# Performance work log

Hardware: AMD Instinct MI355X
Metric: run time of the kernel (lower is better)

The kernel has to match this reference:

```python
import jax, jax.numpy as jnp
import numpy as np

D = 300   # hidden dim (Linear(300,300))
L = 160   # seq len, forced by W3 = Linear(160,1)


def _linear(x, W, b):
    # torch Linear: x @ W.T + b, W is (out, in)
    return jnp.matmul(x, W.T) + b


def setup_inputs() -> dict:
    key = jax.random.key(0)
    ks = jax.random.split(key, 16)
    B = 1024
    s = 1.0 / np.sqrt(D)
    inp = {
        'T_feature': jax.random.normal(ks[0], (B, L, D), jnp.float32),
        'CD_feature': jax.random.normal(ks[1], (B, L, D), jnp.float32),
        'Wproj': jax.random.normal(ks[2], (D, D), jnp.float32) * s,
        'bproj': jnp.zeros((D,), jnp.float32),
        'WqT_w': jax.random.normal(ks[3], (D, D), jnp.float32) * s,
        'WqT_b': jnp.zeros((D,), jnp.float32),
        'WqCD_w': jax.random.normal(ks[4], (D, D), jnp.float32) * s,
        'WqCD_b': jnp.zeros((D,), jnp.float32),
        'WkT_w': jax.random.normal(ks[5], (D, D), jnp.float32) * s,
        'WkT_b': jnp.zeros((D,), jnp.float32),
        'WkCD_w': jax.random.normal(ks[6], (D, D), jnp.float32) * s,
        'WkCD_b': jnp.zeros((D,), jnp.float32),
        'W3_w': jax.random.normal(ks[7], (1, L), jnp.float32) * (1.0 / np.sqrt(L)),
        'W3_b': jnp.zeros((1,), jnp.float32),
    }
    return inp


def reference(T_feature, CD_feature, Wproj, bproj, WqT_w, WqT_b, WqCD_w, WqCD_b,
              WkT_w, WkT_b, WkCD_w, WkCD_b, W3_w, W3_b):
    sqrt_d = jnp.sqrt(jnp.float32(D))
    proj_T = _linear(T_feature, Wproj, bproj)     # (B, L, D)
    proj_CD = _linear(CD_feature, Wproj, bproj)   # (B, L, D)

    # N_tensor @ proj_T is just the mean over tokens (weights 1/Len)
    mean_T = jnp.mean(proj_T, axis=1, keepdims=True)          # (B, 1, D)
    qT = _linear(mean_T, WqT_w, WqT_b)                        # (B, 1, D)
    kT = _linear(proj_T, WkT_w, WkT_b)                        # (B, L, D)
    alphaT = jnp.einsum('bqd,bkd->bqk', qT, kT) / sqrt_d      # (B, 1, L)
    ZT = jax.nn.sigmoid(alphaT)

    qCD = _linear(proj_CD, WqCD_w, WqCD_b)                    # (B, L, D)
    kCD = _linear(proj_CD, WkCD_w, WkCD_b)                    # (B, L, D)
    alphaCD = jnp.einsum('bqd,bkd->bqk', qCD, kCD) / sqrt_d   # (B, L, L)
    ZCD = jax.nn.sigmoid(alphaCD)

    # The per-token loop+cat is a plain broadcast multiply: Mt[:,i,:] = ZCD[:,i,:] * ZT[:,0,:]
    Mt = ZCD * ZT                                             # (B, L, L)
    alpha_f = jax.nn.softmax(_linear(Mt, W3_w, W3_b), axis=1) # (B, L, 1)

    # Second loop is a per-token scalar scale: HCD[:,i,:] = alpha_f[:,i,0] * proj_CD[:,i,:]
    HCD = alpha_f * proj_CD                                   # (B, L, D)
    return (proj_T, HCD)
```

## Files before the change

### kernel.cpp

```cpp
#include <hip/hip_runtime.h>
#include <hip/hip_bf16.h>


typedef __attribute__((ext_vector_type(8))) short short8;
typedef __attribute__((ext_vector_type(4))) float f32x4;

#define DP 320

__device__ __forceinline__ unsigned short f2bf(float x) {
  unsigned int u = __builtin_bit_cast(unsigned int, x);
  u += 0x7FFFu + ((u >> 16) & 1u);
  return (unsigned short)(u >> 16);
}
__device__ __forceinline__ float bf2f(unsigned short h) {
  unsigned int u = ((unsigned int)h) << 16;
  return __builtin_bit_cast(float, u);
}
__device__ __forceinline__ void gload16(const void* g, void* l) {
  __builtin_amdgcn_global_load_lds(
      (const __attribute__((address_space(1))) unsigned int*)g,
      (__attribute__((address_space(3))) unsigned int*)l, 16, 0, 0);
}
__device__ __forceinline__ float sigm(float x) { return 1.0f / (1.0f + __expf(-x)); }

__global__ void wb_k(const float* __restrict__ W, unsigned short* __restrict__ Wb) {
  int n = blockIdx.x, k = threadIdx.x;
  unsigned short v = 0;
  if (n < 300 && k < 300) v = f2bf(W[n * 300 + k]);
  Wb[n * DP + k] = v;
}

__global__ void crossdot_k(const float* __restrict__ Wa, const float* __restrict__ ba,
                           const float* __restrict__ Wc, const float* __restrict__ bc,
                           unsigned short* __restrict__ out_h, float* __restrict__ out_f,
                           float scale) {
  int n = blockIdx.x, c = threadIdx.x;
  float v = 0.f;
  if (n <= 300 && c <= 300) {
    for (int o = 0; o < 300; ++o) {
      float a = (c < 300) ? Wa[o * 300 + c] : ba[o];
      float b = (n < 300) ? Wc[o * 300 + n] : bc[o];
      v += a * b;
    }
    v *= scale;
  }
  if (out_h) out_h[n * DP + c] = f2bf(v);
  else       out_f[n * DP + c] = v;
}

template<int MODE>
__global__ __launch_bounds__(512)
void gemm_k(const float* __restrict__ Af, const unsigned short* __restrict__ Ah,
            const unsigned short* __restrict__ Bsrc, const float* __restrict__ bias,
            float* __restrict__ Of, unsigned short* __restrict__ Oh) {
  __shared__ __align__(16) unsigned short As[2][256 * 32];
  __shared__ __align__(16) unsigned short Bs[2][160 * 32];
  const int tid = threadIdx.x;
  const int wid = tid >> 6, lane = tid & 63;
  const long m0 = (long)blockIdx.y * 256;
  const int n0 = blockIdx.x * 160;

  f32x4 acc[4][5];
#pragma unroll
  for (int i = 0; i < 4; ++i)
#pragma unroll
    for (int j = 0; j < 5; ++j) acc[i][j] = (f32x4){0.f, 0.f, 0.f, 0.f};

  auto stageA = [&](int buf, int k0) {
    if (MODE < 2) {
#pragma unroll
      for (int it = 0; it < 2; ++it) {
        const int row = (tid >> 2) + it * 128;
        const int cg = (tid & 3) * 8;
        const float* p = Af + (m0 + row) * 300 + k0 + cg;
        short8 h;
        if (k0 + cg + 7 < 300) {
          f32x4 x0 = *(const f32x4*)p;
          f32x4 x1 = *(const f32x4*)(p + 4);
#pragma unroll
          for (int j = 0; j < 4; ++j) {
            h[j] = (short)f2bf(x0[j]);
            h[j + 4] = (short)f2bf(x1[j]);
          }
        } else {
#pragma unroll
          for (int j = 0; j < 8; ++j) {
            float v = (k0 + cg + j < 300) ? p[j] : 0.f;
            h[j] = (short)f2bf(v);
          }
        }
        *(short8*)&As[buf][row * 32 + cg] = h;
      }
    } else {
#pragma unroll
      for (int c = 0; c < 2; ++c) {
        int ch = wid + c * 8;
        int f = ch * 512 + lane * 8;
        gload16(Ah + (m0 + (f >> 5)) * DP + k0 + (f & 31), &As[buf][ch * 512]);
      }
    }
  };
  auto stageB = [&](int buf, int k0) {
    {
      int f = wid * 512 + lane * 8;
      gload16(Bsrc + (n0 + (f >> 5)) * DP + k0 + (f & 31), &Bs[buf][wid * 512]);
    }
    if (wid < 2) {
      int ch = wid + 8;
      int f = ch * 512 + lane * 8;
      gload16(Bsrc + (n0 + (f >> 5)) * DP + k0 + (f & 31), &Bs[buf][ch * 512]);
    }
  };

  stageA(0, 0);
  stageB(0, 0);
  __syncthreads();
  int buf = 0;
  const int rm = (wid >> 1) * 64, cn = (wid & 1) * 80;
  const int lr = lane & 15, lk = (lane >> 4) * 8;
  for (int kc = 0; kc < 10; ++kc) {
    if (kc < 9) { stageA(buf ^ 1, (kc + 1) * 32); stageB(buf ^ 1, (kc + 1) * 32); }
    short8 a[4], bb[5];
#pragma unroll
    for (int mf = 0; mf < 4; ++mf)
      a[mf] = *(const short8*)&As[buf][(rm + mf * 16 + lr) * 32 + lk];
#pragma unroll
    for (int nf = 0; nf < 5; ++nf)
      bb[nf] = *(const short8*)&Bs[buf][(cn + nf * 16 + lr) * 32 + lk];
#pragma unroll
    for (int mf = 0; mf < 4; ++mf)
#pragma unroll
      for (int nf = 0; nf < 5; ++nf)
        acc[mf][nf] = __builtin_amdgcn_mfma_f32_16x16x32_bf16(a[mf], bb[nf], acc[mf][nf], 0, 0, 0);
    __syncthreads();
    buf ^= 1;
  }

#pragma unroll
  for (int mf = 0; mf < 4; ++mf) {
#pragma unroll
    for (int nf = 0; nf < 5; ++nf) {
      const int col = n0 + cn + nf * 16 + lr;
      float bv = 0.f;
      if (MODE < 2 && col < 300) bv = bias[col];
#pragma unroll
      for (int r = 0; r < 4; ++r) {
        const long row = m0 + rm + mf * 16 + (lane >> 4) * 4 + r;
        float v = acc[mf][nf][r] + bv;
        if (MODE == 0) {
          if (col < 300) Of[row * 300 + col] = v;
        } else if (MODE == 1) {
          unsigned short u = (col < 300) ? f2bf(v)
                            : ((col == 300) ? f2bf(1.0f) : (unsigned short)0);
          Oh[row * DP + col] = u;
        } else {
          Oh[row * DP + col] = (col <= 300) ? f2bf(v) : (unsigned short)0;
        }
      }
    }
  }
}

__global__ void mean_k(const float* __restrict__ projT, float* __restrict__ meanT) {
  int b = blockIdx.x, tid = threadIdx.x;
  const float* p = projT + (size_t)b * 48000;
  for (int c = tid; c < 300; c += 256) {
    float s = 0.f;
    for (int l = 0; l < 160; ++l) s += p[l * 300 + c];
    meanT[b * DP + c] = s * (1.0f / 160.0f);
  }
}

__global__ __launch_bounds__(320)
void vt_k(const float* __restrict__ Pmat, const float* __restrict__ meanT,
          float* __restrict__ vT, float* __restrict__ cT) {
  __shared__ float mt[300];
  int b = blockIdx.x, tid = threadIdx.x;
  if (tid < 300) mt[tid] = meanT[b * DP + tid];
  __syncthreads();
  if (tid <= 300) {
    float s = 0.f;
    for (int a = 0; a < 300; ++a) s += Pmat[a * DP + tid] * mt[a];
    s += Pmat[300 * DP + tid];
    if (tid < 300) vT[b * DP + tid] = s;
    else cT[b] = s;
  }
}

__global__ __launch_bounds__(256)
void zt_k(const float* __restrict__ projT, const float* __restrict__ vT,
          const float* __restrict__ cT, float* __restrict__ ZT) {
  __shared__ float v[304];
  int b = blockIdx.x, tid = threadIdx.x, wid = tid >> 6, lane = tid & 63;
  for (int c = tid; c < 300; c += 256) v[c] = vT[b * DP + c];
  if (tid == 0) v[300] = cT[b];
  __syncthreads();
  const float* p = projT + (size_t)b * 48000;
  for (int j = wid; j < 160; j += 4) {
    const float* row = p + j * 300;
    float s = 0.f;
    for (int c = lane; c < 300; c += 64) s += v[c] * row[c];
#pragma unroll
    for (int m = 1; m < 64; m <<= 1) s += __shfl_xor(s, m, 64);
    if (lane == 0) ZT[b * 160 + j] = sigm(s + v[300]);
  }
}

__global__ __launch_bounds__(320)
void finale_k(const unsigned short* __restrict__ Y, const unsigned short* __restrict__ P,
              const float* __restrict__ ZT, const float* __restrict__ W3w,
              float* __restrict__ out) {
  __shared__ __align__(16) unsigned short Ys[2][160 * 32];
  __shared__ __align__(16) unsigned short Ps[2][160 * 32];
  __shared__ float t_arr[160];
  __shared__ float s_arr[160];
  __shared__ float red0;

  const int b = blockIdx.x;
  const int tid = threadIdx.x, wid = tid >> 6, lane = tid & 63;
  const unsigned short* Yb = Y + (size_t)b * 160 * DP;
  const unsigned short* Pb = P + (size_t)b * 160 * DP;

  if (tid < 160) t_arr[tid] = ZT[b * 160 + tid] * W3w[tid];

  auto stage = [&](int buf, int k0) {
#pragma unroll
    for (int c = 0; c < 2; ++c) {
      int ch = wid + c * 5;
      int f = ch * 512 + lane * 8;
      int ro = (f >> 5) * DP + k0 + (f & 31);
      gload16(Yb + ro, &Ys[buf][ch * 512]);
      gload16(Pb + ro, &Ps[buf][ch * 512]);
    }
  };

  f32x4 acc[2][10];
#pragma unroll
  for (int i = 0; i < 2; ++i)
#pragma unroll
    for (int j = 0; j < 10; ++j) acc[i][j] = (f32x4){0.f, 0.f, 0.f, 0.f};

  stage(0, 0);
  __syncthreads();
  int buf = 0;
  const int lr = lane & 15, lk = (lane >> 4) * 8;
  const int rm = wid * 32;
  for (int kc = 0; kc < 10; ++kc) {
    if (kc < 9) stage(buf ^ 1, (kc + 1) * 32);
    short8 a[2], bb[10];
#pragma unroll
    for (int mf = 0; mf < 2; ++mf)
      a[mf] = *(const short8*)&Ys[buf][(rm + mf * 16 + lr) * 32 + lk];
#pragma unroll
    for (int nf = 0; nf < 10; ++nf)
      bb[nf] = *(const short8*)&Ps[buf][(nf * 16 + lr) * 32 + lk];
#pragma unroll
    for (int mf = 0; mf < 2; ++mf)
#pragma unroll
      for (int nf = 0; nf < 10; ++nf)
        acc[mf][nf] = __builtin_amdgcn_mfma_f32_16x16x32_bf16(a[mf], bb[nf], acc[mf][nf], 0, 0, 0);
    __syncthreads();
    buf ^= 1;
  }

  float tv[10];
#pragma unroll
  for (int nf = 0; nf < 10; ++nf) tv[nf] = t_arr[nf * 16 + lr];
  float rp[2][4];
#pragma unroll
  for (int mf = 0; mf < 2; ++mf)
#pragma unroll
    for (int r = 0; r < 4; ++r) {
      float s = 0.f;
#pragma unroll
      for (int nf = 0; nf < 10; ++nf) s += sigm(acc[mf][nf][r]) * tv[nf];
      rp[mf][r] = s;
    }
#pragma unroll
  for (int m = 1; m < 16; m <<= 1)
#pragma unroll
    for (int mf = 0; mf < 2; ++mf)
#pragma unroll
      for (int r = 0; r < 4; ++r) rp[mf][r] += __shfl_xor(rp[mf][r], m, 64);
  if (lr == 0) {
#pragma unroll
    for (int mf = 0; mf < 2; ++mf)
#pragma unroll
      for (int r = 0; r < 4; ++r)
        s_arr[rm + mf * 16 + (lane >> 4) * 4 + r] = rp[mf][r];
  }
  __syncthreads();
  if (wid == 0) {
    float v0 = s_arr[lane], v1 = s_arr[lane + 64];
    float v2 = (lane < 32) ? s_arr[lane + 128] : -3.0e38f;
    float mx = fmaxf(fmaxf(v0, v1), v2);
#pragma unroll
    for (int m = 1; m < 64; m <<= 1) mx = fmaxf(mx, __shfl_xor(mx, m, 64));
    float e0 = __expf(v0 - mx), e1 = __expf(v1 - mx);
    float e2 = (lane < 32) ? __expf(v2 - mx) : 0.f;
    s_arr[lane] = e0; s_arr[lane + 64] = e1;
    if (lane < 32) s_arr[lane + 128] = e2;
    float sm = e0 + e1 + e2;
#pragma unroll
    for (int m = 1; m < 64; m <<= 1) sm += __shfl_xor(sm, m, 64);
    if (lane == 0) red0 = 1.0f / sm;
  }
  __syncthreads();
  const float inv = red0;
  float* ob = out + (size_t)b * 48000;
  for (int e = tid; e < 48000; e += 320) {
    const int i = e / 300;
    const int c = e - i * 300;
    ob[e] = s_arr[i] * inv * bf2f(Pb[i * DP + c]);
  }
}

extern "C" void kernel_launch(void* const* d_in, const int* in_sizes, int n_in,
                              void* d_out, int out_size, void* d_ws, size_t ws_size,
                              hipStream_t stream) {
  (void)in_sizes; (void)n_in; (void)out_size; (void)ws_size;
  const float* T      = (const float*)d_in[0];
  const float* CD     = (const float*)d_in[1];
  const float* Wproj  = (const float*)d_in[2];
  const float* bproj  = (const float*)d_in[3];
  const float* WqT_w  = (const float*)d_in[4];
  const float* WqT_b  = (const float*)d_in[5];
  const float* WqCD_w = (const float*)d_in[6];
  const float* WqCD_b = (const float*)d_in[7];
  const float* WkT_w  = (const float*)d_in[8];
  const float* WkT_b  = (const float*)d_in[9];
  const float* WkCD_w = (const float*)d_in[10];
  const float* WkCD_b = (const float*)d_in[11];
  const float* W3_w   = (const float*)d_in[12];

  char* ws = (char*)d_ws;
  size_t off = 0;
  auto alloc = [&](size_t bytes) { void* p = ws + off; off = (off + bytes + 255) & ~(size_t)255; return p; };
  unsigned short* pCD   = (unsigned short*)alloc((size_t)1024 * 160 * DP * 2);
  unsigned short* Yb    = (unsigned short*)alloc((size_t)1024 * 160 * DP * 2);
  unsigned short* Wb    = (unsigned short*)alloc((size_t)DP * DP * 2);
  unsigned short* MaugT = (unsigned short*)alloc((size_t)DP * DP * 2);
  float* Pmat  = (float*)alloc((size_t)DP * DP * 4);
  float* meanT = (float*)alloc((size_t)1024 * DP * 4);
  float* vT    = (float*)alloc((size_t)1024 * DP * 4);
  float* cT    = (float*)alloc((size_t)1024 * 4);
  float* ZT    = (float*)alloc((size_t)1024 * 160 * 4);

  float* projT = (float*)d_out;
  float* HCD   = (float*)d_out + (size_t)49152000;

  const float isd = 1.0f / sqrtf(300.0f);

  wb_k<<<dim3(320), dim3(320), 0, stream>>>(Wproj, Wb);
  crossdot_k<<<dim3(320), dim3(320), 0, stream>>>(WqCD_w, WqCD_b, WkCD_w, WkCD_b, MaugT, nullptr, isd);
  crossdot_k<<<dim3(320), dim3(320), 0, stream>>>(WkT_w, WkT_b, WqT_w, WqT_b, nullptr, Pmat, isd);

  gemm_k<0><<<dim3(2, 640), dim3(512), 0, stream>>>(T,  nullptr, Wb, bproj, projT, nullptr);
  gemm_k<1><<<dim3(2, 640), dim3(512), 0, stream>>>(CD, nullptr, Wb, bproj, nullptr, pCD);

  mean_k<<<dim3(1024), dim3(256), 0, stream>>>(projT, meanT);
  vt_k<<<dim3(1024), dim3(320), 0, stream>>>(Pmat, meanT, vT, cT);
  zt_k<<<dim3(1024), dim3(256), 0, stream>>>(projT, vT, cT, ZT);

  gemm_k<2><<<dim3(2, 640), dim3(512), 0, stream>>>(nullptr, pCD, MaugT, nullptr, nullptr, Yb);

  finale_k<<<dim3(1024), dim3(320), 0, stream>>>(Yb, pCD, ZT, W3_w, HCD);
}
```

Before: 773.7 us.

## Fuse Y=P·M GEMM into finale, merge projection GEMMs and gate kernels

Drops the separate gemm_k<2> that wrote Y (bf16 pCD·Maug) to global memory. finale_k now keeps the whole per-batch pCD tile in swizzled LDS and computes Y in chunks on the fly before the second MFMA, which removes a large global write and re-read. The two projection GEMMs are merged into one launch that covers the full N=320 width per block with padded LDS rows. mean, vT and ZT are fused into a single gate_k. The cost is heavy LDS use (~130KB) in finale and lower occupancy, plus redundant recomputation of the Maug operand loads per batch.

```diff
diff --git a/kernel.cpp b/kernel.cpp
--- a/kernel.cpp
+++ b/kernel.cpp
@@ -22,6 +22,8 @@
       (__attribute__((address_space(3))) unsigned int*)l, 16, 0, 0);
 }
 __device__ __forceinline__ float sigm(float x) { return 1.0f / (1.0f + __expf(-x)); }
+__device__ __forceinline__ int swz640(int row, int g) { return row * 640 + ((g ^ (row & 7)) << 4); }
+__device__ __forceinline__ int swzY(int row, int g) { return row * 128 + ((g ^ (row & 7)) << 4); }
 
 __global__ void wb_k(const float* __restrict__ W, unsigned short* __restrict__ Wb) {
   int n = blockIdx.x, k = threadIdx.x;
@@ -48,17 +50,18 @@
   else       out_f[n * DP + c] = v;
 }
 
-template<int MODE>
 __global__ __launch_bounds__(512)
-void gemm_k(const float* __restrict__ Af, const unsigned short* __restrict__ Ah,
-            const unsigned short* __restrict__ Bsrc, const float* __restrict__ bias,
+void gemm_k(const float* __restrict__ Tsrc, const float* __restrict__ CDsrc,
+            const unsigned short* __restrict__ Wb, const float* __restrict__ bias,
             float* __restrict__ Of, unsigned short* __restrict__ Oh) {
-  __shared__ __align__(16) unsigned short As[2][256 * 32];
-  __shared__ __align__(16) unsigned short Bs[2][160 * 32];
-  const int tid = threadIdx.x;
-  const int wid = tid >> 6, lane = tid & 63;
-  const long m0 = (long)blockIdx.y * 256;
-  const int n0 = blockIdx.x * 160;
+  __shared__ __align__(16) unsigned short As[2][128 * 40];
+  __shared__ __align__(16) unsigned short Bs[2][320 * 40];
+  const int tid = threadIdx.x, wid = tid >> 6, lane = tid & 63;
+  const int mode = blockIdx.y;
+  const float* __restrict__ A = mode ? CDsrc : Tsrc;
+  const long m0 = (long)blockIdx.x * 128;
+  const int lr = lane & 15, lk = (lane >> 4) * 8;
+  const int rm = (wid >> 2) * 64, cn = (wid & 3) * 80;
 
   f32x4 acc[4][5];
 #pragma unroll
@@ -67,66 +70,46 @@
     for (int j = 0; j < 5; ++j) acc[i][j] = (f32x4){0.f, 0.f, 0.f, 0.f};
 
   auto stageA = [&](int buf, int k0) {
-    if (MODE < 2) {
-#pragma unroll
-      for (int it = 0; it < 2; ++it) {
-        const int row = (tid >> 2) + it * 128;
-        const int cg = (tid & 3) * 8;
-        const float* p = Af + (m0 + row) * 300 + k0 + cg;
-        short8 h;
-        if (k0 + cg + 7 < 300) {
-          f32x4 x0 = *(const f32x4*)p;
-          f32x4 x1 = *(const f32x4*)(p + 4);
-#pragma unroll
-          for (int j = 0; j < 4; ++j) {
-            h[j] = (short)f2bf(x0[j]);
-            h[j + 4] = (short)f2bf(x1[j]);
-          }
-        } else {
-#pragma unroll
-          for (int j = 0; j < 8; ++j) {
-            float v = (k0 + cg + j < 300) ? p[j] : 0.f;
-            h[j] = (short)f2bf(v);
-          }
-        }
-        *(short8*)&As[buf][row * 32 + cg] = h;
+    const int row = tid >> 2, cg = (tid & 3) * 8;
+    const float* p = A + (m0 + row) * 300 + k0 + cg;
+    short8 h;
+    if (k0 + cg + 8 <= 300) {
+      f32x4 x0 = *(const f32x4*)p, x1 = *(const f32x4*)(p + 4);
+#pragma unroll
+      for (int j = 0; j < 4; ++j) { h[j] = (short)f2bf(x0[j]); h[j + 4] = (short)f2bf(x1[j]); }
+    } else {
+#pragma unroll
+      for (int j = 0; j < 8; ++j) {
+        float v = (k0 + cg + j < 300) ? p[j] : 0.f;
+        h[j] = (short)f2bf(v);
       }
-    } else {
-#pragma unroll
-      for (int c = 0; c < 2; ++c) {
-        int ch = wid + c * 8;
-        int f = ch * 512 + lane * 8;
-        gload16(Ah + (m0 + (f >> 5)) * DP + k0 + (f & 31), &As[buf][ch * 512]);
-      }
-    }
+    }
+    *(short8*)&As[buf][row * 40 + cg] = h;
   };
   auto stageB = [&](int buf, int k0) {
-    {
-      int f = wid * 512 + lane * 8;
-      gload16(Bsrc + (n0 + (f >> 5)) * DP + k0 + (f & 31), &Bs[buf][wid * 512]);
-    }
-    if (wid < 2) {
-      int ch = wid + 8;
-      int f = ch * 512 + lane * 8;
-      gload16(Bsrc + (n0 + (f >> 5)) * DP + k0 + (f & 31), &Bs[buf][ch * 512]);
+#pragma unroll
+    for (int it = 0; it < 3; ++it) {
+      int idx = tid + it * 512;
+      if (idx < 1280) {
+        int row = idx >> 2, cg = (idx & 3) * 8;
+        short8 h = *(const short8*)(Wb + row * DP + k0 + cg);
+        *(short8*)&Bs[buf][row * 40 + cg] = h;
+      }
     }
   };
 
-  stageA(0, 0);
-  stageB(0, 0);
+  stageA(0, 0); stageB(0, 0);
   __syncthreads();
   int buf = 0;
-  const int rm = (wid >> 1) * 64, cn = (wid & 1) * 80;
-  const int lr = lane & 15, lk = (lane >> 4) * 8;
   for (int kc = 0; kc < 10; ++kc) {
     if (kc < 9) { stageA(buf ^ 1, (kc + 1) * 32); stageB(buf ^ 1, (kc + 1) * 32); }
     short8 a[4], bb[5];
 #pragma unroll
     for (int mf = 0; mf < 4; ++mf)
-      a[mf] = *(const short8*)&As[buf][(rm + mf * 16 + lr) * 32 + lk];
+      a[mf] = *(const short8*)&As[buf][(rm + mf * 16 + lr) * 40 + lk];
 #pragma unroll
     for (int nf = 0; nf < 5; ++nf)
-      bb[nf] = *(const short8*)&Bs[buf][(cn + nf * 16 + lr) * 32 + lk];
+      bb[nf] = *(const short8*)&Bs[buf][(cn + nf * 16 + lr) * 40 + lk];
 #pragma unroll
     for (int mf = 0; mf < 4; ++mf)
 #pragma unroll
@@ -137,158 +120,170 @@
   }
 
 #pragma unroll
-  for (int mf = 0; mf < 4; ++mf) {
+  for (int mf = 0; mf < 4; ++mf)
 #pragma unroll
     for (int nf = 0; nf < 5; ++nf) {
-      const int col = n0 + cn + nf * 16 + lr;
-      float bv = 0.f;
-      if (MODE < 2 && col < 300) bv = bias[col];
+      const int col = cn + nf * 16 + lr;
+      const float bv = (col < 300) ? bias[col] : 0.f;
 #pragma unroll
       for (int r = 0; r < 4; ++r) {
         const long row = m0 + rm + mf * 16 + (lane >> 4) * 4 + r;
         float v = acc[mf][nf][r] + bv;
-        if (MODE == 0) {
+        if (mode == 0) {
           if (col < 300) Of[row * 300 + col] = v;
-        } else if (MODE == 1) {
+        } else {
           unsigned short u = (col < 300) ? f2bf(v)
                             : ((col == 300) ? f2bf(1.0f) : (unsigned short)0);
           Oh[row * DP + col] = u;
-        } else {
-          Oh[row * DP + col] = (col <= 300) ? f2bf(v) : (unsigned short)0;
         }
       }
     }
-  }
-}
-
-__global__ void mean_k(const float* __restrict__ projT, float* __restrict__ meanT) {
-  int b = blockIdx.x, tid = threadIdx.x;
+}
+
+__global__ __launch_bounds__(320)
+void gate_k(const float* __restrict__ projT, const float* __restrict__ Pmat,
+            float* __restrict__ ZT) {
+  __shared__ float mt[304];
+  __shared__ float vv[304];
+  const int b = blockIdx.x, tid = threadIdx.x, wid = tid >> 6, lane = tid & 63;
   const float* p = projT + (size_t)b * 48000;
-  for (int c = tid; c < 300; c += 256) {
+  if (tid < 300) {
     float s = 0.f;
-    for (int l = 0; l < 160; ++l) s += p[l * 300 + c];
-    meanT[b * DP + c] = s * (1.0f / 160.0f);
-  }
-}
-
-__global__ __launch_bounds__(320)
-void vt_k(const float* __restrict__ Pmat, const float* __restrict__ meanT,
-          float* __restrict__ vT, float* __restrict__ cT) {
-  __shared__ float mt[300];
-  int b = blockIdx.x, tid = threadIdx.x;
-  if (tid < 300) mt[tid] = meanT[b * DP + tid];
+#pragma unroll 4
+    for (int l = 0; l < 160; ++l) s += p[l * 300 + tid];
+    mt[tid] = s * (1.0f / 160.0f);
+  }
   __syncthreads();
   if (tid <= 300) {
-    float s = 0.f;
+    float s = Pmat[300 * DP + tid];
     for (int a = 0; a < 300; ++a) s += Pmat[a * DP + tid] * mt[a];
-    s += Pmat[300 * DP + tid];
-    if (tid < 300) vT[b * DP + tid] = s;
-    else cT[b] = s;
-  }
-}
-
-__global__ __launch_bounds__(256)
-void zt_k(const float* __restrict__ projT, const float* __restrict__ vT,
-          const float* __restrict__ cT, float* __restrict__ ZT) {
-  __shared__ float v[304];
-  int b = blockIdx.x, tid = threadIdx.x, wid = tid >> 6, lane = tid & 63;
-  for (int c = tid; c < 300; c += 256) v[c] = vT[b * DP + c];
-  if (tid == 0) v[300] = cT[b];
-  __syncthreads();
-  const float* p = projT + (size_t)b * 48000;
-  for (int j = wid; j < 160; j += 4) {
+    vv[tid] = s;
+  }
+  __syncthreads();
+  for (int j = wid * 32; j < wid * 32 + 32; ++j) {
     const float* row = p + j * 300;
     float s = 0.f;
-    for (int c = lane; c < 300; c += 64) s += v[c] * row[c];
+    for (int c = lane; c < 300; c += 64) s += vv[c] * row[c];
 #pragma unroll
     for (int m = 1; m < 64; m <<= 1) s += __shfl_xor(s, m, 64);
-    if (lane == 0) ZT[b * 160 + j] = sigm(s + v[300]);
-  }
-}
-
-__global__ __launch_bounds__(320)
-void finale_k(const unsigned short* __restrict__ Y, const unsigned short* __restrict__ P,
+    if (lane == 0) ZT[b * 160 + j] = sigm(s + vv[300]);
+  }
+}
+
+__global__ __launch_bounds__(640)
+void finale_k(const unsigned short* __restrict__ P, const unsigned short* __restrict__ Maug,
               const float* __restrict__ ZT, const float* __restrict__ W3w,
               float* __restrict__ out) {
-  __shared__ __align__(16) unsigned short Ys[2][160 * 32];
-  __shared__ __align__(16) unsigned short Ps[2][160 * 32];
+  __shared__ __align__(16) unsigned short Ps[160 * 320];
+  __shared__ __align__(16) unsigned short Ms[32 * 320];
+  __shared__ __align__(16) unsigned short Ys[160 * 64];
   __shared__ float t_arr[160];
+  __shared__ float s_part[5][160];
   __shared__ float s_arr[160];
   __shared__ float red0;
 
-  const int b = blockIdx.x;
-  const int tid = threadIdx.x, wid = tid >> 6, lane = tid & 63;
-  const unsigned short* Yb = Y + (size_t)b * 160 * DP;
+  const int b = blockIdx.x, tid = threadIdx.x, wid = tid >> 6, lane = tid & 63;
+  const int lr = lane & 15, hi = lane >> 4;
   const unsigned short* Pb = P + (size_t)b * 160 * DP;
 
   if (tid < 160) t_arr[tid] = ZT[b * 160 + tid] * W3w[tid];
 
-  auto stage = [&](int buf, int k0) {
-#pragma unroll
-    for (int c = 0; c < 2; ++c) {
-      int ch = wid + c * 5;
-      int f = ch * 512 + lane * 8;
-      int ro = (f >> 5) * DP + k0 + (f & 31);
-      gload16(Yb + ro, &Ys[buf][ch * 512]);
-      gload16(Pb + ro, &Ps[buf][ch * 512]);
-    }
-  };
-
-  f32x4 acc[2][10];
-#pragma unroll
-  for (int i = 0; i < 2; ++i)
-#pragma unroll
-    for (int j = 0; j < 10; ++j) acc[i][j] = (f32x4){0.f, 0.f, 0.f, 0.f};
-
-  stage(0, 0);
-  __syncthreads();
-  int buf = 0;
-  const int lr = lane & 15, lk = (lane >> 4) * 8;
-  const int rm = wid * 32;
-  for (int kc = 0; kc < 10; ++kc) {
-    if (kc < 9) stage(buf ^ 1, (kc + 1) * 32);
-    short8 a[2], bb[10];
-#pragma unroll
-    for (int mf = 0; mf < 2; ++mf)
-      a[mf] = *(const short8*)&Ys[buf][(rm + mf * 16 + lr) * 32 + lk];
-#pragma unroll
-    for (int nf = 0; nf < 10; ++nf)
-      bb[nf] = *(const short8*)&Ps[buf][(nf * 16 + lr) * 32 + lk];
-#pragma unroll
-    for (int mf = 0; mf < 2; ++mf)
-#pragma unroll
-      for (int nf = 0; nf < 10; ++nf)
-        acc[mf][nf] = __builtin_amdgcn_mfma_f32_16x16x32_bf16(a[mf], bb[nf], acc[mf][nf], 0, 0, 0);
+#pragma unroll
+  for (int it = 0; it < 10; ++it) {
+    int o = it * 640 + tid;
+    int row = o / 40, g = o - row * 40;
+    gload16(Pb + row * DP + ((g ^ (row & 7)) << 3),
+            (char*)Ps + ((it * 640 + (wid << 6)) << 4));
+  }
+  short8 mreg[2];
+  int mrow[2], mg[2];
+#pragma unroll
+  for (int it = 0; it < 2; ++it) {
+    int idx = tid + it * 640;
+    mrow[it] = idx / 40; mg[it] = idx - mrow[it] * 40;
+    mreg[it] = *(const short8*)(Maug + mrow[it] * DP + mg[it] * 8);
+  }
+  __syncthreads();
+#pragma unroll
+  for (int it = 0; it < 2; ++it)
+    *(short8*)((char*)Ms + swz640(mrow[it], mg[it])) = mreg[it];
+  short8 a_pre[10];
+#pragma unroll
+  for (int kk = 0; kk < 10; ++kk)
+    a_pre[kk] = *(const short8*)((const char*)Ps + swz640(16 * wid + lr, kk * 4 + hi));
+  __syncthreads();
+
+  f32x4 acc_s[5][2];
+#pragma unroll
+  for (int i = 0; i < 5; ++i)
+#pragma unroll
+    for (int j = 0; j < 2; ++j) acc_s[i][j] = (f32x4){0.f, 0.f, 0.f, 0.f};
+  const int wm = wid / 5, wn = wid - wm * 5;
+
+  for (int nc = 0; nc < 10; ++nc) {
+    if (nc < 9) {
+#pragma unroll
+      for (int it = 0; it < 2; ++it)
+        mreg[it] = *(const short8*)(Maug + ((nc + 1) * 32 + mrow[it]) * DP + mg[it] * 8);
+    }
+    f32x4 accy0 = (f32x4){0.f, 0.f, 0.f, 0.f}, accy1 = accy0;
+#pragma unroll
+    for (int kk = 0; kk < 10; ++kk) {
+      short8 b0 = *(const short8*)((const char*)Ms + swz640(lr, kk * 4 + hi));
+      short8 b1 = *(const short8*)((const char*)Ms + swz640(16 + lr, kk * 4 + hi));
+      accy0 = __builtin_amdgcn_mfma_f32_16x16x32_bf16(a_pre[kk], b0, accy0, 0, 0, 0);
+      accy1 = __builtin_amdgcn_mfma_f32_16x16x32_bf16(a_pre[kk], b1, accy1, 0, 0, 0);
+    }
     __syncthreads();
-    buf ^= 1;
-  }
-
-  float tv[10];
-#pragma unroll
-  for (int nf = 0; nf < 10; ++nf) tv[nf] = t_arr[nf * 16 + lr];
-  float rp[2][4];
-#pragma unroll
-  for (int mf = 0; mf < 2; ++mf)
 #pragma unroll
     for (int r = 0; r < 4; ++r) {
-      float s = 0.f;
-#pragma unroll
-      for (int nf = 0; nf < 10; ++nf) s += sigm(acc[mf][nf][r]) * tv[nf];
-      rp[mf][r] = s;
-    }
+      int row = 16 * wid + hi * 4 + r;
+      int c0 = lr, c1 = 16 + lr;
+      *(unsigned short*)((char*)Ys + swzY(row, c0 >> 3) + ((c0 & 7) << 1)) = f2bf(accy0[r]);
+      *(unsigned short*)((char*)Ys + swzY(row, c1 >> 3) + ((c1 & 7) << 1)) = f2bf(accy1[r]);
+    }
+    if (nc < 9) {
+#pragma unroll
+      for (int it = 0; it < 2; ++it)
+        *(short8*)((char*)Ms + swz640(mrow[it], mg[it])) = mreg[it];
+    }
+    __syncthreads();
+#pragma unroll
+    for (int mf = 0; mf < 5; ++mf) {
+      short8 a = *(const short8*)((const char*)Ys + swzY(80 * wm + mf * 16 + lr, hi));
+#pragma unroll
+      for (int nf = 0; nf < 2; ++nf) {
+        short8 bv = *(const short8*)((const char*)Ps + swz640(32 * wn + nf * 16 + lr, nc * 4 + hi));
+        acc_s[mf][nf] = __builtin_amdgcn_mfma_f32_16x16x32_bf16(a, bv, acc_s[mf][nf], 0, 0, 0);
+      }
+    }
+    __syncthreads();
+  }
+
+  float tv0 = t_arr[32 * wn + lr], tv1 = t_arr[32 * wn + 16 + lr];
+  float pp[5][4];
+#pragma unroll
+  for (int mf = 0; mf < 5; ++mf)
+#pragma unroll
+    for (int r = 0; r < 4; ++r)
+      pp[mf][r] = sigm(acc_s[mf][0][r]) * tv0 + sigm(acc_s[mf][1][r]) * tv1;
 #pragma unroll
   for (int m = 1; m < 16; m <<= 1)
 #pragma unroll
-    for (int mf = 0; mf < 2; ++mf)
-#pragma unroll
-      for (int r = 0; r < 4; ++r) rp[mf][r] += __shfl_xor(rp[mf][r], m, 64);
+    for (int mf = 0; mf < 5; ++mf)
+#pragma unroll
+      for (int r = 0; r < 4; ++r)
+        pp[mf][r] += __shfl_xor(pp[mf][r], m, 64);
   if (lr == 0) {
 #pragma unroll
-    for (int mf = 0; mf < 2; ++mf)
+    for (int mf = 0; mf < 5; ++mf)
 #pragma unroll
       for (int r = 0; r < 4; ++r)
-        s_arr[rm + mf * 16 + (lane >> 4) * 4 + r] = rp[mf][r];
-  }
+        s_part[wn][80 * wm + mf * 16 + hi * 4 + r] = pp[mf][r];
+  }
+  __syncthreads();
+  if (tid < 160)
+    s_arr[tid] = s_part[0][tid] + s_part[1][tid] + s_part[2][tid] + s_part[3][tid] + s_part[4][tid];
   __syncthreads();
   if (wid == 0) {
     float v0 = s_arr[lane], v1 = s_arr[lane + 64];
@@ -308,10 +303,10 @@
   __syncthreads();
   const float inv = red0;
   float* ob = out + (size_t)b * 48000;
-  for (int e = tid; e < 48000; e += 320) {
-    const int i = e / 300;
-    const int c = e - i * 300;
-    ob[e] = s_arr[i] * inv * bf2f(Pb[i * DP + c]);
+  for (int e = tid; e < 48000; e += 640) {
+    int i = e / 300, c = e - i * 300;
+    unsigned short pv = *(const unsigned short*)((const char*)Ps + swz640(i, c >> 3) + ((c & 7) << 1));
+    ob[e] = s_arr[i] * inv * bf2f(pv);
   }
 }
 
@@ -337,14 +332,10 @@
   size_t off = 0;
   auto alloc = [&](size_t bytes) { void* p = ws + off; off = (off + bytes + 255) & ~(size_t)255; return p; };
   unsigned short* pCD   = (unsigned short*)alloc((size_t)1024 * 160 * DP * 2);
-  unsigned short* Yb    = (unsigned short*)alloc((size_t)1024 * 160 * DP * 2);
   unsigned short* Wb    = (unsigned short*)alloc((size_t)DP * DP * 2);
   unsigned short* MaugT = (unsigned short*)alloc((size_t)DP * DP * 2);
-  float* Pmat  = (float*)alloc((size_t)DP * DP * 4);
-  float* meanT = (float*)alloc((size_t)1024 * DP * 4);
-  float* vT    = (float*)alloc((size_t)1024 * DP * 4);
-  float* cT    = (float*)alloc((size_t)1024 * 4);
-  float* ZT    = (float*)alloc((size_t)1024 * 160 * 4);
+  float* Pmat = (float*)alloc((size_t)DP * DP * 4);
+  float* ZT   = (float*)alloc((size_t)1024 * 160 * 4);
 
   float* projT = (float*)d_out;
   float* HCD   = (float*)d_out + (size_t)49152000;
@@ -355,14 +346,7 @@
   crossdot_k<<<dim3(320), dim3(320), 0, stream>>>(WqCD_w, WqCD_b, WkCD_w, WkCD_b, MaugT, nullptr, isd);
   crossdot_k<<<dim3(320), dim3(320), 0, stream>>>(WkT_w, WkT_b, WqT_w, WqT_b, nullptr, Pmat, isd);
 
-  gemm_k<0><<<dim3(2, 640), dim3(512), 0, stream>>>(T,  nullptr, Wb, bproj, projT, nullptr);
-  gemm_k<1><<<dim3(2, 640), dim3(512), 0, stream>>>(CD, nullptr, Wb, bproj, nullptr, pCD);
-
-  mean_k<<<dim3(1024), dim3(256), 0, stream>>>(projT, meanT);
-  vt_k<<<dim3(1024), dim3(320), 0, stream>>>(Pmat, meanT, vT, cT);
-  zt_k<<<dim3(1024), dim3(256), 0, stream>>>(projT, vT, cT, ZT);
-
-  gemm_k<2><<<dim3(2, 640), dim3(512), 0, stream>>>(nullptr, pCD, MaugT, nullptr, nullptr, Yb);
-
-  finale_k<<<dim3(1024), dim3(320), 0, stream>>>(Yb, pCD, ZT, W3_w, HCD);
-}
+  gemm_k<<<dim3(1280, 2), dim3(512), 0, stream>>>(T, CD, Wb, bproj, projT, pCD);
+  gate_k<<<dim3(1024), dim3(320), 0, stream>>>(projT, Pmat, ZT);
+  finale_k<<<dim3(1024), dim3(640), 0, stream>>>(pCD, MaugT, ZT, W3_w, HCD);
+}
```

Result: faster. 627.4 us (-18.9%).
